# Performance work log

Hardware: AMD Instinct MI355X
Metric: run time of the kernel (lower is better)

## Reference

```python
import jax, jax.numpy as jnp
import numpy as np

P = 16        # patch size
WIN = 64      # attention window size
NH = 12       # num heads


def _layernorm(x, g, b, eps=1e-5):
    m = x.mean(-1, keepdims=True)
    v = ((x - m) ** 2).mean(-1, keepdims=True)
    return (x - m) * jax.lax.rsqrt(v + eps) * g + b


def _sinusoidal_pe(n, d):
    pos = jnp.arange(n, dtype=jnp.float32)[:, None]
    i = jnp.arange(d // 2, dtype=jnp.float32)[None, :]
    ang = pos / jnp.power(10000.0, (2.0 * i) / d)
    pe = jnp.zeros((n, d), jnp.float32)
    pe = pe.at[:, 0::2].set(jnp.sin(ang)).at[:, 1::2].set(jnp.cos(ang))
    return pe


def setup_inputs() -> dict:
    key = jax.random.key(0)
    ks = jax.random.split(key, 8)
    B, C, H, W, D, F = 16, 3, 512, 512, 768, 3072
    s = lambda k, shape: (jax.random.normal(k, shape, jnp.float32) * 0.02)
    return {
        "input": jax.random.normal(ks[0], (B, C, H, W), jnp.float32),
        "patch_w": s(ks[1], (D, C, P, P)),
        "patch_b": jnp.zeros((D,), jnp.float32),
        "ln_g": jnp.ones((D,), jnp.float32),
        "ln_b": jnp.zeros((D,), jnp.float32),
        "qkv_w": s(ks[2], (D, 3 * D)),
        "qkv_b": jnp.zeros((3 * D,), jnp.float32),
        "proj_w": s(ks[3], (D, D)),
        "proj_b": jnp.zeros((D,), jnp.float32),
        "ff1_w": s(ks[4], (D, F)),
        "ff1_b": jnp.zeros((F,), jnp.float32),
        "ff2_w": s(ks[5], (F, D)),
        "ff2_b": jnp.zeros((D,), jnp.float32),
    }


def reference(input, patch_w, patch_b, ln_g, ln_b, qkv_w, qkv_b,
              proj_w, proj_b, ff1_w, ff1_b, ff2_w, ff2_b):
    B, C, H, W = input.shape
    D = patch_w.shape[0]
    dh = D // NH
    # --- patch embedding (conv k=stride=P as einsum) + norm ---
    xp = input.reshape(B, C, H // P, P, W // P, P)
    x = jnp.einsum('bchpwq,dcpq->bhwd', xp, patch_w) + patch_b  # [B,32,32,D]
    x = x.reshape(B, -1, D)                                      # [B,N,D]
    x = _layernorm(x, ln_g, ln_b)
    N = x.shape[1]
    # --- static sinusoidal position embedding ---
    x = x + _sinusoidal_pe(N, D)

    def ff(y):  # shared feedforward (dropout=eval/off)
        return jax.nn.gelu(y @ ff1_w + ff1_b) @ ff2_w + ff2_b

    def sparse_attn(y):  # windowed block-sparse attention, window=64
        nW = N // WIN
        qkv = (y @ qkv_w + qkv_b).reshape(B, nW, WIN, 3, NH, dh)
        q, k, v = qkv[:, :, :, 0], qkv[:, :, :, 1], qkv[:, :, :, 2]
        scores = jnp.einsum('bwqhd,bwkhd->bwhqk', q, k) * (dh ** -0.5)
        a = jax.nn.softmax(scores, axis=-1)
        o = jnp.einsum('bwhqk,bwkhd->bwqhd', a, v).reshape(B, N, D)
        return o @ proj_w + proj_b

    identity = x
    x = ff(x)
    x = sparse_attn(x)
    x = x + identity
    identity = x
    x = ff(x)
    x = x + identity
    return x
```

## Files before the change

### kernel.cpp

```cpp
#include <hip/hip_runtime.h>

typedef unsigned int uint;
typedef short bf16x8 __attribute__((ext_vector_type(8)));
typedef float f32x4 __attribute__((ext_vector_type(4)));

__device__ __forceinline__ unsigned short f2b(float f) {
    uint u = __builtin_bit_cast(uint, f);
    u += 0x7fffu + ((u >> 16) & 1u);
    return (unsigned short)(u >> 16);
}
__device__ __forceinline__ float b2f(unsigned short h) {
    uint u = ((uint)h) << 16;
    return __builtin_bit_cast(float, u);
}

__device__ __forceinline__ float fast_gelu(float v) {
    float s  = v * v;
    float t2 = __builtin_fmaf(0.044715f * s, v, v);
    float e  = __expf(-1.5957691216f * t2);
    return v * __builtin_amdgcn_rcpf(1.0f + e);
}

__device__ __forceinline__ void gl_lds16(const unsigned short* g, unsigned short* l) {
    __builtin_amdgcn_global_load_lds(
        reinterpret_cast<const __attribute__((address_space(1))) unsigned int*>(
            reinterpret_cast<uintptr_t>(g)),
        reinterpret_cast<__attribute__((address_space(3))) unsigned int*>(
            reinterpret_cast<uintptr_t>(l)),
        16, 0, 0);
}

__global__ __launch_bounds__(256) void convert_bf16_kernel(const float* __restrict__ src,
                                                           unsigned short* __restrict__ dst, int n) {
    int idx = blockIdx.x * 256 + threadIdx.x;
    if (idx < n) dst[idx] = f2b(src[idx]);
}

__global__ __launch_bounds__(256) void transpose_to_bf16_kernel(const float* __restrict__ src,
                                                                unsigned short* __restrict__ dst,
                                                                int K, int N) {
    long long idx = (long long)blockIdx.x * 256 + threadIdx.x;
    if (idx >= (long long)K * N) return;
    int k = (int)(idx / N);
    int n = (int)(idx % N);
    dst[(long long)n * K + k] = f2b(src[idx]);
}

__global__ __launch_bounds__(256) void im2col_kernel(const float* __restrict__ in,
                                                     unsigned short* __restrict__ out) {
    long long idx = (long long)blockIdx.x * 256 + threadIdx.x;
    int k = (int)(idx % 768);
    int n = (int)(idx / 768);
    int b = n >> 10, t = n & 1023;
    int hp = t >> 5, wp = t & 31;
    int c = k >> 8, rm = k & 255;
    int p = rm >> 4, q = rm & 15;
    long long src = (((long long)(b * 3 + c) * 512) + hp * 16 + p) * 512 + wp * 16 + q;
    out[idx] = f2b(in[src]);
}

__global__ __launch_bounds__(256) void ln_pe_kernel(const float* __restrict__ xe,
                                                    const float* __restrict__ g,
                                                    const float* __restrict__ bb,
                                                    unsigned short* __restrict__ xb) {
    int row = blockIdx.x;
    int pos = row & 1023;
    const float* xr = xe + (long long)row * 768;
    float v0 = xr[threadIdx.x];
    float v1 = xr[threadIdx.x + 256];
    float v2 = xr[threadIdx.x + 512];
    float s = v0 + v1 + v2;
    float sq = v0 * v0 + v1 * v1 + v2 * v2;
    for (int o = 32; o > 0; o >>= 1) {
        s  += __shfl_down(s, o, 64);
        sq += __shfl_down(sq, o, 64);
    }
    __shared__ float ps[4], pq[4];
    int w = threadIdx.x >> 6, lane = threadIdx.x & 63;
    if (lane == 0) { ps[w] = s; pq[w] = sq; }
    __syncthreads();
    float ts = ps[0] + ps[1] + ps[2] + ps[3];
    float tq = pq[0] + pq[1] + pq[2] + pq[3];
    float mean = ts * (1.0f / 768.0f);
    float var  = tq * (1.0f / 768.0f) - mean * mean;
    float inv  = rsqrtf(var + 1e-5f);
    #pragma unroll
    for (int dd = 0; dd < 3; dd++) {
        int d = threadIdx.x + dd * 256;
        float val = (dd == 0) ? v0 : (dd == 1) ? v1 : v2;
        float y = (val - mean) * inv * g[d] + bb[d];
        float freq = __expf(-(float)(d & ~1) * (9.210340371976184f / 768.0f));
        float ang = (float)pos * freq;
        y += (d & 1) ? cosf(ang) : sinf(ang);
        xb[(long long)row * 768 + d] = f2b(y);
    }
}

__global__ __launch_bounds__(512) void gemm256_kernel(const unsigned short* __restrict__ A,
                                                      const unsigned short* __restrict__ BT,
                                                      const float* __restrict__ bias,
                                                      const unsigned short* __restrict__ residB,
                                                      float* __restrict__ outF,
                                                      unsigned short* __restrict__ outB,
                                                      int M, int N, int K, int ldb,
                                                      int epi, int accumF) {
    __shared__ __align__(16) unsigned short As[2][256 * 64];
    __shared__ __align__(16) unsigned short Bs[2][256 * 64];

    const int nX = N >> 8;
    int id = blockIdx.x;
    int xcd = id & 7;
    int sq_ = id >> 3;
    int bx = sq_ % nX;
    int by = (sq_ / nX) * 8 + xcd;
    const int m0 = by * 256, n0 = bx * 256;

    const int tid = threadIdx.x;
    const int w = tid >> 6, lane = tid & 63;
    const int wr = w >> 2, wc = w & 3;
    const int quad = lane >> 4, l15 = lane & 15;
    const int swz = l15 & 7;

    const int row0 = tid >> 3;
    const int c8   = tid & 7;
    const int gc8  = c8 ^ (row0 & 7);
    const unsigned short* Ag = A  + (long long)(m0 + row0) * K   + gc8 * 8;
    const unsigned short* Bg = BT + (long long)(n0 + row0) * ldb + gc8 * 8;
    unsigned short* Ad = &As[0][0] + row0 * 64 + c8 * 8;
    unsigned short* Bd = &Bs[0][0] + row0 * 64 + c8 * 8;
    const long long aK64 = (long long)64 * K,  aK128 = (long long)128 * K;
    const long long bL64 = (long long)64 * ldb, bL128 = (long long)128 * ldb;

#define STAGE_A(bsel, h, ks) { \
    const unsigned short* s_ = Ag + (h) * aK128 + (ks); \
    unsigned short* d_ = Ad + (bsel) * 16384 + (h) * 8192; \
    gl_lds16(s_, d_); gl_lds16(s_ + aK64, d_ + 4096); }
#define STAGE_B(bsel, h, ks) { \
    const unsigned short* s_ = Bg + (h) * bL128 + (ks); \
    unsigned short* d_ = Bd + (bsel) * 16384 + (h) * 8192; \
    gl_lds16(s_, d_); gl_lds16(s_ + bL64, d_ + 4096); }

    bf16x8 af[4][2], bfr[2][2];
    f32x4 acc[2][2][4][2] = {};

#define LOAD_AF(bsel, qm) { \
    const unsigned short* base_ = &As[bsel][((qm) * 128 + wr * 64 + l15) * 64]; \
    _Pragma("unroll") for (int mf_ = 0; mf_ < 4; mf_++) { \
      af[mf_][0] = *(const bf16x8*)(base_ + mf_ * 1024 + ((quad ^ swz) * 8)); \
      af[mf_][1] = *(const bf16x8*)(base_ + mf_ * 1024 + (((4 + quad) ^ swz) * 8)); \
    } }
#define LOAD_BF(bsel, qn) { \
    const unsigned short* base_ = &Bs[bsel][((qn) * 128 + wc * 32 + l15) * 64]; \
    _Pragma("unroll") for (int nf_ = 0; nf_ < 2; nf_++) { \
      bfr[nf_][0] = *(const bf16x8*)(base_ + nf_ * 1024 + ((quad ^ swz) * 8)); \
      bfr[nf_][1] = *(const bf16x8*)(base_ + nf_ * 1024 + (((4 + quad) ^ swz) * 8)); \
    } }
#define MFMA_Q(qm, qn) { \
    __builtin_amdgcn_sched_barrier(0); \
    __builtin_amdgcn_s_setprio(1); \
    _Pragma("unroll") for (int mf_ = 0; mf_ < 4; mf_++) \
    _Pragma("unroll") for (int nf_ = 0; nf_ < 2; nf_++) { \
      acc[qm][qn][mf_][nf_] = __builtin_amdgcn_mfma_f32_16x16x32_bf16(af[mf_][0], bfr[nf_][0], acc[qm][qn][mf_][nf_], 0, 0, 0); \
      acc[qm][qn][mf_][nf_] = __builtin_amdgcn_mfma_f32_16x16x32_bf16(af[mf_][1], bfr[nf_][1], acc[qm][qn][mf_][nf_], 0, 0, 0); \
    } \
    __builtin_amdgcn_s_setprio(0); \
    __builtin_amdgcn_sched_barrier(0); }
#define BAR() { asm volatile("" ::: "memory"); __builtin_amdgcn_s_barrier(); asm volatile("" ::: "memory"); }

    const int NT = K >> 6;

    STAGE_B(0, 0, 0);
    STAGE_A(0, 0, 0);
    STAGE_B(0, 1, 0);
    STAGE_A(0, 1, 0);
    STAGE_A(1, 0, 64);
    STAGE_B(1, 1, 64);
    STAGE_A(1, 1, 64);
    asm volatile("s_waitcnt vmcnt(6)" ::: "memory");
    BAR();

    for (int s = 0; s < NT; s++) {
        const int b = s & 1, bn = b ^ 1;
        const int ks1 = (s + 1 < NT) ? (s + 1) * 64 : 0;
        const int ks2 = (s + 2 < NT) ? (s + 2) * 64 : 0;

        LOAD_AF(b, 0);
        LOAD_BF(b, 0);
        STAGE_B(bn, 0, ks1);
        asm volatile("s_waitcnt lgkmcnt(8)" ::: "memory");
        BAR();
        MFMA_Q(0, 0);
        BAR();
        LOAD_BF(b, 1);
        STAGE_A(b, 0, ks2);
        BAR();
        MFMA_Q(0, 1);
        BAR();
        LOAD_AF(b, 1);
        STAGE_B(b, 1, ks2);
        BAR();
        MFMA_Q(1, 1);
        BAR();
        LOAD_BF(b, 0);
        STAGE_A(b, 1, ks2);
        BAR();
        MFMA_Q(1, 0);
        asm volatile("s_waitcnt vmcnt(6)" ::: "memory");
        BAR();
    }
    asm volatile("s_waitcnt vmcnt(0)" ::: "memory");

    const int r0 = quad * 4;
    #pragma unroll
    for (int qm = 0; qm < 2; qm++)
    #pragma unroll
    for (int qn = 0; qn < 2; qn++)
    #pragma unroll
    for (int mf = 0; mf < 4; mf++)
    #pragma unroll
    for (int nf = 0; nf < 2; nf++) {
        int gn = n0 + qn * 128 + wc * 32 + nf * 16 + l15;
        float bv = bias ? bias[gn] : 0.0f;
        #pragma unroll
        for (int r = 0; r < 4; r++) {
            int gm = m0 + qm * 128 + wr * 64 + mf * 16 + r0 + r;
            float v = acc[qm][qn][mf][nf][r] + bv;
            if (epi == 1) v = fast_gelu(v);
            long long off = (long long)gm * N + gn;
            if (accumF) v += outF[off];
            if (residB) v += b2f(residB[off]);
            if (outF) outF[off] = v;
            if (outB) outB[off] = f2b(v);
        }
    }
#undef STAGE_A
#undef STAGE_B
#undef LOAD_AF
#undef LOAD_BF
#undef MFMA_Q
#undef BAR
}

__global__ __launch_bounds__(256) void attn_kernel(const unsigned short* __restrict__ qkv,
                                                   unsigned short* __restrict__ o) {
    __shared__ float qs[64 * 65], ks[64 * 65], vs[64 * 65];
    __shared__ float pmax[4 * 64], psum[4 * 64];
    int blk = blockIdx.x;
    int h = blk % 12;
    int bw = blk / 12;
    int wi = bw % 16, b = bw / 16;
    int rowBase = b * 1024 + wi * 64;
    int tid = threadIdx.x;

    int lr = tid >> 2, c0 = (tid & 3) * 16;
    const unsigned short* src = qkv + (long long)(rowBase + lr) * 2304 + h * 64 + c0;
    #pragma unroll
    for (int j = 0; j < 16; j++) {
        qs[lr * 65 + c0 + j] = b2f(src[j]);
        ks[lr * 65 + c0 + j] = b2f(src[768 + j]);
        vs[lr * 65 + c0 + j] = b2f(src[1536 + j]);
    }
    __syncthreads();

    int r = tid & 63, cg = tid >> 6;
    float svals[16] = {};
    for (int kk = 0; kk < 64; kk++) {
        float qv = qs[r * 65 + kk];
        #pragma unroll
        for (int j = 0; j < 16; j++)
            svals[j] += qv * ks[(cg * 16 + j) * 65 + kk];
    }
    float smax = -1e30f;
    #pragma unroll
    for (int j = 0; j < 16; j++) {
        svals[j] *= 0.125f;
        smax = fmaxf(smax, svals[j]);
    }
    pmax[cg * 64 + r] = smax;
    __syncthreads();
    float m = fmaxf(fmaxf(pmax[r], pmax[64 + r]), fmaxf(pmax[128 + r], pmax[192 + r]));
    float lsum = 0.0f;
    #pragma unroll
    for (int j = 0; j < 16; j++) {
        float e = __expf(svals[j] - m);
        qs[r * 65 + cg * 16 + j] = e;
        lsum += e;
    }
    psum[cg * 64 + r] = lsum;
    __syncthreads();
    float inv = __builtin_amdgcn_rcpf(psum[r] + psum[64 + r] + psum[128 + r] + psum[192 + r]);

    float oacc[16] = {};
    for (int c = 0; c < 64; c++) {
        float pv = qs[r * 65 + c];
        #pragma unroll
        for (int j = 0; j < 16; j++)
            oacc[j] += pv * vs[c * 65 + cg * 16 + j];
    }
    unsigned short* dst = o + (long long)(rowBase + r) * 768 + h * 64 + cg * 16;
    #pragma unroll
    for (int j = 0; j < 16; j++) dst[j] = f2b(oacc[j] * inv);
}

extern "C" void kernel_launch(void* const* d_in, const int* in_sizes, int n_in,
                              void* d_out, int out_size, void* d_ws, size_t ws_size,
                              hipStream_t stream) {
    const float* input   = (const float*)d_in[0];
    const float* patch_w = (const float*)d_in[1];
    const float* patch_b = (const float*)d_in[2];
    const float* ln_g    = (const float*)d_in[3];
    const float* ln_b    = (const float*)d_in[4];
    const float* qkv_w   = (const float*)d_in[5];
    const float* qkv_b   = (const float*)d_in[6];
    const float* proj_w  = (const float*)d_in[7];
    const float* proj_b  = (const float*)d_in[8];
    const float* ff1_w   = (const float*)d_in[9];
    const float* ff1_b   = (const float*)d_in[10];
    const float* ff2_w   = (const float*)d_in[11];
    const float* ff2_b   = (const float*)d_in[12];
    float* out = (float*)d_out;

    const int MN = 16384;
    const int D = 768, F = 3072, TD = 2304;
    const int NY = MN / 256;

    unsigned short* wPatch = (unsigned short*)d_ws;
    unsigned short* wQkvT  = wPatch + 589824;
    unsigned short* wProjT = wQkvT + 1769472;
    unsigned short* wFf1T  = wProjT + 589824;
    unsigned short* wFf2T  = wFf1T + 2359296;
    unsigned short* bigBuf = wFf2T + 2359296;
    unsigned short* xid    = bigBuf + 50331648;
    unsigned short* t0     = xid + 12582912;

    convert_bf16_kernel<<<(589824 + 255) / 256, 256, 0, stream>>>(patch_w, wPatch, 589824);
    transpose_to_bf16_kernel<<<(1769472 + 255) / 256, 256, 0, stream>>>(qkv_w, wQkvT, D, TD);
    transpose_to_bf16_kernel<<<(589824 + 255) / 256, 256, 0, stream>>>(proj_w, wProjT, D, D);
    transpose_to_bf16_kernel<<<(2359296 + 255) / 256, 256, 0, stream>>>(ff1_w, wFf1T, D, F);
    transpose_to_bf16_kernel<<<(2359296 + 255) / 256, 256, 0, stream>>>(ff2_w, wFf2T, F, D);

    im2col_kernel<<<(MN * 768) / 256, 256, 0, stream>>>(input, bigBuf);

    gemm256_kernel<<<(D / 256) * NY, 512, 0, stream>>>(bigBuf, wPatch, patch_b, nullptr,
                                                       out, nullptr, MN, D, 768, 768, 0, 0);
    ln_pe_kernel<<<MN, 256, 0, stream>>>(out, ln_g, ln_b, xid);

    gemm256_kernel<<<(F / 256) * NY, 512, 0, stream>>>(xid, wFf1T, ff1_b, nullptr,
                                                       nullptr, bigBuf, MN, F, 768, 768, 1, 0);
    gemm256_kernel<<<(D / 256) * NY, 512, 0, stream>>>(bigBuf, wFf2T, ff2_b, nullptr,
                                                       nullptr, t0, MN, D, F, F, 0, 0);
    gemm256_kernel<<<(TD / 256) * NY, 512, 0, stream>>>(t0, wQkvT, qkv_b, nullptr,
                                                        nullptr, bigBuf, MN, TD, 768, 768, 0, 0);
    attn_kernel<<<16 * 16 * 12, 256, 0, stream>>>(bigBuf, t0);

    gemm256_kernel<<<(D / 256) * NY, 512, 0, stream>>>(t0, wProjT, proj_b, xid,
                                                       nullptr, xid, MN, D, 768, 768, 0, 0);

    gemm256_kernel<<<(F / 256) * NY, 512, 0, stream>>>(xid, wFf1T, ff1_b, nullptr,
                                                       nullptr, bigBuf, MN, F, 768, 768, 1, 0);
    gemm256_kernel<<<(D / 256) * NY, 512, 0, stream>>>(bigBuf, wFf2T, ff2_b, xid,
                                                       out, nullptr, MN, D, F, F, 0, 0);
}
```

Before: 940.0 us.

## Double-buffer MFMA fragments with inline-asm LDS reads and cross-iteration prefetch

The GEMM main loop now keeps two sets of A and B register fragments and issues the LDS reads through inline-asm ds_read_b128 with immediate offsets from precomputed base addresses. The next iteration's first fragments are prefetched during the last MFMA quadrant by flipping the buffer bit in the address registers. Explicit lgkmcnt and vmcnt waits replace the previous waits so LDS reads overlap with MFMA work. This raises register pressure and depends on hand-tuned waitcnt values being correct alongside the global-to-LDS staging.

```diff
diff --git a/kernel.cpp b/kernel.cpp
--- a/kernel.cpp
+++ b/kernel.cpp
@@ -140,32 +140,46 @@
     unsigned short* d_ = Bd + (bsel) * 16384 + (h) * 8192; \
     gl_lds16(s_, d_); gl_lds16(s_ + bL64, d_ + 4096); }
 
-    bf16x8 af[4][2], bfr[2][2];
+    unsigned asB = (unsigned)(uintptr_t)(&As[0][0]);
+    unsigned bsB = (unsigned)(uintptr_t)(&Bs[0][0]);
+    unsigned aH0 = asB + (unsigned)((wr * 64 + l15) * 128 + ((quad ^ swz) * 16));
+    unsigned aH1 = asB + (unsigned)((wr * 64 + l15) * 128 + (((4 + quad) ^ swz) * 16));
+    unsigned bH0 = bsB + (unsigned)((wc * 32 + l15) * 128 + ((quad ^ swz) * 16));
+    unsigned bH1 = bsB + (unsigned)((wc * 32 + l15) * 128 + (((4 + quad) ^ swz) * 16));
+
+    bf16x8 afA[4][2], afB[4][2], bfr0[2][2], bfr1[2][2];
     f32x4 acc[2][2][4][2] = {};
 
-#define LOAD_AF(bsel, qm) { \
-    const unsigned short* base_ = &As[bsel][((qm) * 128 + wr * 64 + l15) * 64]; \
-    _Pragma("unroll") for (int mf_ = 0; mf_ < 4; mf_++) { \
-      af[mf_][0] = *(const bf16x8*)(base_ + mf_ * 1024 + ((quad ^ swz) * 8)); \
-      af[mf_][1] = *(const bf16x8*)(base_ + mf_ * 1024 + (((4 + quad) ^ swz) * 8)); \
-    } }
-#define LOAD_BF(bsel, qn) { \
-    const unsigned short* base_ = &Bs[bsel][((qn) * 128 + wc * 32 + l15) * 64]; \
-    _Pragma("unroll") for (int nf_ = 0; nf_ < 2; nf_++) { \
-      bfr[nf_][0] = *(const bf16x8*)(base_ + nf_ * 1024 + ((quad ^ swz) * 8)); \
-      bfr[nf_][1] = *(const bf16x8*)(base_ + nf_ * 1024 + (((4 + quad) ^ swz) * 8)); \
-    } }
-#define MFMA_Q(qm, qn) { \
+#define DSR(dst, addr, IMM) \
+    asm volatile("ds_read_b128 %0, %1 offset:%2" : "=&v"(dst) : "v"(addr), "i"(IMM))
+
+#define R_A0() { DSR(afA[0][0], aH0, 0);     DSR(afA[1][0], aH0, 2048); \
+                 DSR(afA[2][0], aH0, 4096);  DSR(afA[3][0], aH0, 6144); \
+                 DSR(afA[0][1], aH1, 0);     DSR(afA[1][1], aH1, 2048); \
+                 DSR(afA[2][1], aH1, 4096);  DSR(afA[3][1], aH1, 6144); }
+#define R_A1() { DSR(afB[0][0], aH0, 16384); DSR(afB[1][0], aH0, 18432); \
+                 DSR(afB[2][0], aH0, 20480); DSR(afB[3][0], aH0, 22528); \
+                 DSR(afB[0][1], aH1, 16384); DSR(afB[1][1], aH1, 18432); \
+                 DSR(afB[2][1], aH1, 20480); DSR(afB[3][1], aH1, 22528); }
+#define R_B0() { DSR(bfr0[0][0], bH0, 0);     DSR(bfr0[1][0], bH0, 2048); \
+                 DSR(bfr0[0][1], bH1, 0);     DSR(bfr0[1][1], bH1, 2048); }
+#define R_B1() { DSR(bfr1[0][0], bH0, 16384); DSR(bfr1[1][0], bH0, 18432); \
+                 DSR(bfr1[0][1], bH1, 16384); DSR(bfr1[1][1], bH1, 18432); }
+
+#define MFMA16(AF, BF, qm, qn) { \
     __builtin_amdgcn_sched_barrier(0); \
     __builtin_amdgcn_s_setprio(1); \
     _Pragma("unroll") for (int mf_ = 0; mf_ < 4; mf_++) \
     _Pragma("unroll") for (int nf_ = 0; nf_ < 2; nf_++) { \
-      acc[qm][qn][mf_][nf_] = __builtin_amdgcn_mfma_f32_16x16x32_bf16(af[mf_][0], bfr[nf_][0], acc[qm][qn][mf_][nf_], 0, 0, 0); \
-      acc[qm][qn][mf_][nf_] = __builtin_amdgcn_mfma_f32_16x16x32_bf16(af[mf_][1], bfr[nf_][1], acc[qm][qn][mf_][nf_], 0, 0, 0); \
+      acc[qm][qn][mf_][nf_] = __builtin_amdgcn_mfma_f32_16x16x32_bf16(AF[mf_][0], BF[nf_][0], acc[qm][qn][mf_][nf_], 0, 0, 0); \
+      acc[qm][qn][mf_][nf_] = __builtin_amdgcn_mfma_f32_16x16x32_bf16(AF[mf_][1], BF[nf_][1], acc[qm][qn][mf_][nf_], 0, 0, 0); \
     } \
     __builtin_amdgcn_s_setprio(0); \
     __builtin_amdgcn_sched_barrier(0); }
+
 #define BAR() { asm volatile("" ::: "memory"); __builtin_amdgcn_s_barrier(); asm volatile("" ::: "memory"); }
+#define WAITL(n) { asm volatile("s_waitcnt lgkmcnt(" #n ")" ::: "memory"); __builtin_amdgcn_sched_barrier(0); }
+#define WAITV(n) { asm volatile("s_waitcnt vmcnt(" #n ")" ::: "memory"); }
 
     const int NT = K >> 6;
 
@@ -176,39 +190,43 @@
     STAGE_A(1, 0, 64);
     STAGE_B(1, 1, 64);
     STAGE_A(1, 1, 64);
-    asm volatile("s_waitcnt vmcnt(6)" ::: "memory");
+    WAITV(6);
     BAR();
+    R_A0();
+    R_B0();
 
     for (int s = 0; s < NT; s++) {
         const int b = s & 1, bn = b ^ 1;
         const int ks1 = (s + 1 < NT) ? (s + 1) * 64 : 0;
         const int ks2 = (s + 2 < NT) ? (s + 2) * 64 : 0;
 
-        LOAD_AF(b, 0);
-        LOAD_BF(b, 0);
+        R_B1();
         STAGE_B(bn, 0, ks1);
-        asm volatile("s_waitcnt lgkmcnt(8)" ::: "memory");
-        BAR();
-        MFMA_Q(0, 0);
-        BAR();
-        LOAD_BF(b, 1);
+        BAR();
+        WAITL(4);
+        MFMA16(afA, bfr0, 0, 0);
+        BAR();
+        R_A1();
         STAGE_A(b, 0, ks2);
         BAR();
-        MFMA_Q(0, 1);
-        BAR();
-        LOAD_AF(b, 1);
+        WAITL(8);
+        MFMA16(afA, bfr1, 0, 1);
+        BAR();
         STAGE_B(b, 1, ks2);
         BAR();
-        MFMA_Q(1, 1);
-        BAR();
-        LOAD_BF(b, 0);
+        WAITL(0);
+        MFMA16(afB, bfr1, 1, 1);
+        WAITV(4);
+        BAR();
+        aH0 ^= 32768u; aH1 ^= 32768u; bH0 ^= 32768u; bH1 ^= 32768u;
+        R_A0();
+        MFMA16(afB, bfr0, 1, 0);
+        R_B0();
         STAGE_A(b, 1, ks2);
         BAR();
-        MFMA_Q(1, 0);
-        asm volatile("s_waitcnt vmcnt(6)" ::: "memory");
-        BAR();
-    }
-    asm volatile("s_waitcnt vmcnt(0)" ::: "memory");
+    }
+    asm volatile("s_waitcnt vmcnt(0) lgkmcnt(0)" ::: "memory");
+    __builtin_amdgcn_sched_barrier(0);
 
     const int r0 = quad * 4;
     #pragma unroll
@@ -235,10 +253,15 @@
     }
 #undef STAGE_A
 #undef STAGE_B
-#undef LOAD_AF
-#undef LOAD_BF
-#undef MFMA_Q
+#undef DSR
+#undef R_A0
+#undef R_A1
+#undef R_B0
+#undef R_B1
+#undef MFMA16
 #undef BAR
+#undef WAITL
+#undef WAITV
 }
 
 __global__ __launch_bounds__(256) void attn_kernel(const unsigned short* __restrict__ qkv,
```

Measured after the change: 932.2 us. Within noise of the previous version (-0.8%).
